# Performance work log

Measured on AMD Instinct MI355X. Metric: run time of the kernel, lower is better.

## Reference

```python
import jax, jax.numpy as jnp
import numpy as np

B, T, C, H = 8, 2048, 1024, 64  # batch, context_length, embedding_dim, head_size


def setup_inputs() -> dict:
    key = jax.random.key(0)
    kx, kq, kk, kv = jax.random.split(key, 4)
    s = C ** -0.5  # linear-init-like scale
    return {
        "x": jax.random.normal(kx, (B, T, C), dtype=jnp.float32),
        "Wq": jax.random.normal(kq, (C, H), dtype=jnp.float32) * s,
        "Wk": jax.random.normal(kk, (C, H), dtype=jnp.float32) * s,
        "Wv": jax.random.normal(kv, (C, H), dtype=jnp.float32) * s,
    }


def reference(x, Wq, Wk, Wv):
    Bx, Tx, _ = x.shape
    q = jnp.einsum('btc,ch->bth', x, Wq)
    k = jnp.einsum('btc,ch->bth', x, Wk)
    v = jnp.einsum('btc,ch->bth', x, Wv)
    scale = k.shape[-1] ** -0.5
    scores = jnp.einsum('bth,bsh->bts', q, k) * scale  # [B, T, T]
    causal = jnp.tril(jnp.ones((Tx, Tx), dtype=bool))
    scores = jnp.where(causal, scores, -jnp.inf)
    weights = jax.nn.softmax(scores, axis=-1)
    # dropout is identity in eval mode
    out = jnp.einsum('bts,bsh->bth', weights, v)  # [B, T, H]
    return out
```

## Files before the change

kernel.cpp:

```cpp
#include <hip/hip_runtime.h>
#include <hip/hip_bf16.h>

#define BB 8
#define TT 2048
#define CC 1024
#define HH 64

typedef float f32x4 __attribute__((ext_vector_type(4)));
typedef float f32x16 __attribute__((ext_vector_type(16)));
typedef short s16x8 __attribute__((ext_vector_type(8)));

static __device__ __forceinline__ unsigned short f2bf(float f) {
    unsigned int u = __float_as_uint(f);
    u = (u + 0x7FFFu + ((u >> 16) & 1u)) >> 16;
    return (unsigned short)u;
}

static __device__ __forceinline__ unsigned cvt_pk_bf16(float lo, float hi) {
    unsigned r;
    asm("v_cvt_pk_bf16_f32 %0, %1, %2" : "=v"(r) : "v"(lo), "v"(hi));
    return r;
}

__global__ __launch_bounds__(256) void wt_kernel(
    const float* __restrict__ Wq, const float* __restrict__ Wk,
    const float* __restrict__ Wv, unsigned short* __restrict__ wTf) {
    const int e8 = blockIdx.x * 256 + threadIdx.x;
    const int lane = e8 & 63;
    const int s = (e8 >> 6) & 31;
    const int n16 = e8 >> 11;
    const int sel = n16 >> 2;
    const float* W = (sel == 0) ? Wq : ((sel == 1) ? Wk : Wv);
    const int h = ((n16 & 3) << 4) + (lane & 15);
    const int cb = s * 32 + ((lane >> 4) << 3);
    s16x8 v;
#pragma unroll
    for (int j = 0; j < 8; ++j) v[j] = (short)f2bf(W[(size_t)(cb + j) * HH + h]);
    *reinterpret_cast<s16x8*>(&wTf[(size_t)e8 * 8]) = v;
}

__global__ __launch_bounds__(256, 2) void qkv_kernel(
    const float* __restrict__ x, const unsigned short* __restrict__ wTf,
    unsigned short* __restrict__ Qf, unsigned short* __restrict__ Kf,
    unsigned short* __restrict__ Vf) {
    __shared__ unsigned short xb[2][32 * 128];
    const int tid = threadIdx.x;
    const int wn = tid >> 6, lane = tid & 63;
    const int lo = lane & 15, hi = lane >> 4;
    const int rb = blockIdx.x * 32;

    const int r0 = tid >> 5;
    const int c4 = (tid & 31) * 4;
    const float* xsrc = &x[(size_t)(rb + r0) * CC + c4];

    const int ab0 = lo * 128, as0 = (lo & 7) << 3;
    const int ab1 = (16 + lo) * 128;

    f32x4 acc[2][3];
#pragma unroll
    for (int m = 0; m < 2; ++m)
#pragma unroll
        for (int n = 0; n < 3; ++n) acc[m][n] = (f32x4){0.f, 0.f, 0.f, 0.f};

    f32x4 pfA[4], pfB[4];
#pragma unroll
    for (int i = 0; i < 4; ++i)
        pfA[i] = *reinterpret_cast<const f32x4*>(xsrc + (size_t)(8 * i) * CC);
#pragma unroll
    for (int i = 0; i < 4; ++i)
        pfB[i] = *reinterpret_cast<const f32x4*>(xsrc + (size_t)(8 * i) * CC + 128);

    s16x8 bv[4][3];
#define BLOAD(SET, SLOT)                                                       \
    {                                                                          \
        _Pragma("unroll")                                                      \
        for (int n = 0; n < 3; ++n)                                            \
            bv[SET][n] = *reinterpret_cast<const s16x8*>(                      \
                &wTf[(((size_t)(wn * 3 + n) * 32 + (SLOT)) * 64 + lane) * 8]); \
    }
    BLOAD(0, 0)
    BLOAD(1, 1)
    BLOAD(2, 2)

#pragma unroll
    for (int c = 0; c < 8; ++c) {
        unsigned short* wb = xb[c & 1];
        {
            const f32x4* pf = (c & 1) ? pfB : pfA;
#pragma unroll
            for (int i = 0; i < 4; ++i) {
                const int rr = r0 + 8 * i;
                ushort4 g;
                g.x = f2bf(pf[i][0]); g.y = f2bf(pf[i][1]);
                g.z = f2bf(pf[i][2]); g.w = f2bf(pf[i][3]);
                *reinterpret_cast<ushort4*>(&wb[rr * 128 + (c4 ^ ((rr & 7) << 3))]) = g;
            }
        }
        __syncthreads();
        if (c < 6) {
            if (c & 1) {
#pragma unroll
                for (int i = 0; i < 4; ++i)
                    pfB[i] = *reinterpret_cast<const f32x4*>(
                        xsrc + (size_t)(8 * i) * CC + (c + 2) * 128);
            } else {
#pragma unroll
                for (int i = 0; i < 4; ++i)
                    pfA[i] = *reinterpret_cast<const f32x4*>(
                        xsrc + (size_t)(8 * i) * CC + (c + 2) * 128);
            }
        }
        const unsigned short* base = xb[c & 1];
#pragma unroll
        for (int kh = 0; kh < 4; ++kh) {
            const int slot = c * 4 + kh;
            if (slot + 3 < 32) BLOAD((slot + 3) & 3, slot + 3)
            const s16x8 a0 = *reinterpret_cast<const s16x8*>(
                &base[ab0 + ((kh * 32 + hi * 8) ^ as0)]);
            const s16x8 a1 = *reinterpret_cast<const s16x8*>(
                &base[ab1 + ((kh * 32 + hi * 8) ^ as0)]);
#pragma unroll
            for (int n = 0; n < 3; ++n) {
                acc[0][n] = __builtin_amdgcn_mfma_f32_16x16x32_bf16(a0, bv[slot & 3][n], acc[0][n], 0, 0, 0);
                acc[1][n] = __builtin_amdgcn_mfma_f32_16x16x32_bf16(a1, bv[slot & 3][n], acc[1][n], 0, 0, 0);
            }
        }
    }
#undef BLOAD

    __syncthreads();
    unsigned short* fr = reinterpret_cast<unsigned short*>(xb);
#pragma unroll
    for (int n = 0; n < 3; ++n) {
        const int n16 = wn * 3 + n;
        const int sel = n16 >> 2;
#pragma unroll
        for (int m = 0; m < 2; ++m) {
#pragma unroll
            for (int r = 0; r < 4; ++r) {
                const int tok31 = m * 16 + 4 * hi + r;
                const unsigned short bvv = f2bf(acc[m][n][r]);
                if (sel == 0) {
                    const int s = n16, half = (lo >> 3) & 1, j = lo & 7;
                    fr[(s * 64 + half * 32 + tok31) * 8 + j] = bvv;
                } else if (sel == 1) {
                    const int s = n16 - 4, half = (lo >> 3) & 1, j = lo & 7;
                    fr[2048 + (s * 64 + half * 32 + tok31) * 8 + j] = bvv;
                } else {
                    const int h = (n16 - 8) * 16 + lo;
                    const int mt = h >> 5;
                    const int s2 = tok31 >> 4, hf = (tok31 >> 3) & 1, jj = tok31 & 7;
                    fr[4096 + ((mt * 2 + s2) * 64 + hf * 32 + (h & 31)) * 8 + jj] = bvv;
                }
            }
        }
    }
    __syncthreads();
    const int b_ = rb >> 11;
    const int tile = (rb & (TT - 1)) >> 5;
    const size_t tb = ((size_t)b_ * 64 + tile) * 2048;
#pragma unroll
    for (int i = 0; i < 3; ++i) {
        const int g = tid + 256 * i;
        const int buf = g >> 8;
        const int off = g & 255;
        const s16x8 val = *reinterpret_cast<const s16x8*>(&fr[buf * 2048 + off * 8]);
        unsigned short* dst = (buf == 0) ? Qf : ((buf == 1) ? Kf : Vf);
        *reinterpret_cast<s16x8*>(&dst[tb + off * 8]) = val;
    }
}

__global__ __launch_bounds__(512, 4) void attn_kernel(
    const unsigned short* __restrict__ Qf, const unsigned short* __restrict__ Kf,
    const unsigned short* __restrict__ Vf, float* __restrict__ out) {
    __shared__ __align__(16) char smem[33792 + 2048];
    float (*OfL)[64][33] = reinterpret_cast<float(*)[64][33]>(smem);
    float (*Mm)[32] = reinterpret_cast<float(*)[32]>(smem + 33792);
    float (*Ml)[32] = reinterpret_cast<float(*)[32]>(smem + 33792 + 1024);

    const int tid = threadIdx.x;
    const int wv = tid >> 6, lane = tid & 63;
    const int q = lane & 31, half = lane >> 5;
    const int b = blockIdx.x & 7;
    const int qt = 63 - (blockIdx.x >> 3);
    const int qbase = qt * 32;
    const float CEXP = 0.125f * 1.44269504f;

    const unsigned short* qp = &Qf[(((size_t)b * 64 + qt) * 256 + lane) * 8];
    s16x8 qf[4];
#pragma unroll
    for (int s = 0; s < 4; ++s) qf[s] = *reinterpret_cast<const s16x8*>(qp + s * 512);

    f32x16 oA, oB;
#pragma unroll
    for (int r = 0; r < 16; ++r) { oA[r] = 0.f; oB[r] = 0.f; }
    float m = -1e30f, l = 0.f;

    for (int t = wv; t <= qt; t += 8) {
        const unsigned short* vp = &Vf[(((size_t)b * 64 + t) * 256 + lane) * 8];
        s16x8 vf[4];
#pragma unroll
        for (int i = 0; i < 4; ++i)
            vf[i] = *reinterpret_cast<const s16x8*>(vp + i * 512);
        const unsigned short* kp = &Kf[(((size_t)b * 64 + t) * 256 + lane) * 8];
        f32x16 sa;
#pragma unroll
        for (int r = 0; r < 16; ++r) sa[r] = 0.f;
#pragma unroll
        for (int s = 0; s < 4; ++s) {
            const s16x8 kf = *reinterpret_cast<const s16x8*>(kp + s * 512);
            sa = __builtin_amdgcn_mfma_f32_32x32x16_bf16(kf, qf[s], sa, 0, 0, 0);
        }
        if (t == qt) {
#pragma unroll
            for (int r = 0; r < 16; ++r) {
                const int key = 4 * half + (r & 3) + 8 * (r >> 2);
                if (key > q) sa[r] = -1e30f;
            }
        }
        float pmax = sa[0];
#pragma unroll
        for (int r = 1; r < 16; ++r) pmax = fmaxf(pmax, sa[r]);
        pmax = fmaxf(pmax, __shfl_xor(pmax, 32));
        if (!__all(pmax <= m + 64.f)) {
            const float mnew = fmaxf(m, pmax);
            const float alpha = exp2f((m - mnew) * CEXP);
            l *= alpha;
#pragma unroll
            for (int r = 0; r < 16; ++r) { oA[r] *= alpha; oB[r] *= alpha; }
            m = mnew;
        }
        float rs = 0.f;
#pragma unroll
        for (int r = 0; r < 16; ++r) {
            const float p = exp2f((sa[r] - m) * CEXP);
            sa[r] = p;
            rs += p;
        }
        l += rs + __shfl_xor(rs, 32);
        unsigned d[8];
#pragma unroll
        for (int i = 0; i < 8; ++i) d[i] = cvt_pk_bf16(sa[2 * i], sa[2 * i + 1]);
        const unsigned snd0 = half ? d[0] : d[2];
        const unsigned snd1 = half ? d[1] : d[3];
        const unsigned snd2 = half ? d[4] : d[6];
        const unsigned snd3 = half ? d[5] : d[7];
        const unsigned rcv0 = __shfl_xor(snd0, 32);
        const unsigned rcv1 = __shfl_xor(snd1, 32);
        const unsigned rcv2 = __shfl_xor(snd2, 32);
        const unsigned rcv3 = __shfl_xor(snd3, 32);
        union { unsigned u[4]; s16x8 v; } f0, f1;
        f0.u[0] = half ? rcv0 : d[0];
        f0.u[1] = half ? rcv1 : d[1];
        f0.u[2] = half ? d[2] : rcv0;
        f0.u[3] = half ? d[3] : rcv1;
        f1.u[0] = half ? rcv2 : d[4];
        f1.u[1] = half ? rcv3 : d[5];
        f1.u[2] = half ? d[6] : rcv2;
        f1.u[3] = half ? d[7] : rcv3;
        oA = __builtin_amdgcn_mfma_f32_32x32x16_bf16(vf[0], f0.v, oA, 0, 0, 0);
        oB = __builtin_amdgcn_mfma_f32_32x32x16_bf16(vf[2], f0.v, oB, 0, 0, 0);
        oA = __builtin_amdgcn_mfma_f32_32x32x16_bf16(vf[1], f1.v, oA, 0, 0, 0);
        oB = __builtin_amdgcn_mfma_f32_32x32x16_bf16(vf[3], f1.v, oB, 0, 0, 0);
    }

#define PUBLISH(slot)                                                      \
    {                                                                      \
        _Pragma("unroll")                                                  \
        for (int r = 0; r < 16; ++r) {                                     \
            const int h0 = (r & 3) + 8 * (r >> 2) + 4 * half;              \
            OfL[slot][h0][q] = oA[r];                                      \
            OfL[slot][h0 + 32][q] = oB[r];                                 \
        }                                                                  \
    }
#define MERGE(slot, srcw)                                                  \
    {                                                                      \
        const float mb = Mm[srcw][q], lb = Ml[srcw][q];                    \
        const float M = fmaxf(m, mb);                                      \
        const float wa = exp2f((m - M) * CEXP);                            \
        const float wb = exp2f((mb - M) * CEXP);                           \
        _Pragma("unroll")                                                  \
        for (int r = 0; r < 16; ++r) {                                     \
            const int h0 = (r & 3) + 8 * (r >> 2) + 4 * half;              \
            oA[r] = oA[r] * wa + OfL[slot][h0][q] * wb;                    \
            oB[r] = oB[r] * wa + OfL[slot][h0 + 32][q] * wb;               \
        }                                                                  \
        l = l * wa + lb * wb;                                              \
        m = M;                                                             \
    }

    if (lane < 32) { Mm[wv][q] = m; Ml[wv][q] = l; }
    if (wv >= 4) PUBLISH(wv - 4);
    __syncthreads();
    if (wv < 4) MERGE(wv, wv + 4);
    __syncthreads();
    if (wv == 2 || wv == 3) {
        PUBLISH(wv - 2);
        if (lane < 32) { Mm[wv][q] = m; Ml[wv][q] = l; }
    }
    __syncthreads();
    if (wv < 2) MERGE(wv, wv + 2);
    __syncthreads();
    if (wv == 1) {
        PUBLISH(1);
        if (lane < 32) { Mm[1][q] = m; Ml[1][q] = l; }
    }
    __syncthreads();
    if (wv == 0) {
        MERGE(1, 1);
        const float inv = 1.f / l;
#pragma unroll
        for (int r = 0; r < 16; ++r) {
            const int h0 = (r & 3) + 8 * (r >> 2) + 4 * half;
            OfL[0][h0][q] = oA[r] * inv;
            OfL[0][h0 + 32][q] = oB[r] * inv;
        }
    }
    __syncthreads();
#pragma unroll
    for (int i = 0; i < 4; ++i) {
        const int idx = tid + 512 * i;
        const int h = idx & 63, q2 = idx >> 6;
        out[((size_t)b * TT + qbase + q2) * HH + h] = OfL[0][h][q2];
    }
#undef PUBLISH
#undef MERGE
}

extern "C" void kernel_launch(void* const* d_in, const int* in_sizes, int n_in,
                              void* d_out, int out_size, void* d_ws, size_t ws_size,
                              hipStream_t stream) {
    (void)in_sizes; (void)n_in; (void)out_size; (void)ws_size;
    const float* x  = (const float*)d_in[0];
    const float* Wq = (const float*)d_in[1];
    const float* Wk = (const float*)d_in[2];
    const float* Wv = (const float*)d_in[3];
    float* out = (float*)d_out;

    char* ws = (char*)d_ws;
    unsigned short* wTf = (unsigned short*)ws;
    unsigned short* Qf  = (unsigned short*)(ws + 393216);
    unsigned short* Kf  = (unsigned short*)(ws + 393216 + 2097152);
    unsigned short* Vf  = (unsigned short*)(ws + 393216 + 4194304);

    wt_kernel<<<96, 256, 0, stream>>>(Wq, Wk, Wv, wTf);
    qkv_kernel<<<512, 256, 0, stream>>>(x, wTf, Qf, Kf, Vf);
    attn_kernel<<<512, 512, 0, stream>>>(Qf, Kf, Vf, out);
}
```

Before: 42.35 us.

## Load whole 32x1024 x tile into LDS upfront instead of double-buffered chunks

The QKV projection kernel now loads and converts the block's entire 32-row x slab (64 KB bf16 in LDS) in one pass with a single barrier, then runs all 32 MFMA k-slots without further barriers. This removes the per-chunk register prefetch, double-buffer switching and eight __syncthreads. In exchange, global-load latency is no longer overlapped with MFMA work, and the much larger LDS footprint may cut the number of resident blocks per CU below the launch-bounds target of 2.

```diff
diff --git a/kernel.cpp b/kernel.cpp
--- a/kernel.cpp
+++ b/kernel.cpp
@@ -43,32 +43,33 @@
     const float* __restrict__ x, const unsigned short* __restrict__ wTf,
     unsigned short* __restrict__ Qf, unsigned short* __restrict__ Kf,
     unsigned short* __restrict__ Vf) {
-    __shared__ unsigned short xb[2][32 * 128];
+    __shared__ unsigned short xt[32 * 1024];
     const int tid = threadIdx.x;
     const int wn = tid >> 6, lane = tid & 63;
     const int lo = lane & 15, hi = lane >> 4;
     const int rb = blockIdx.x * 32;
 
-    const int r0 = tid >> 5;
-    const int c4 = (tid & 31) * 4;
-    const float* xsrc = &x[(size_t)(rb + r0) * CC + c4];
-
-    const int ab0 = lo * 128, as0 = (lo & 7) << 3;
-    const int ab1 = (16 + lo) * 128;
+#pragma unroll
+    for (int i = 0; i < 16; ++i) {
+        const int gid = tid + 256 * i;
+        const int row = gid >> 7, g = gid & 127;
+        const float* src = &x[(size_t)(rb + row) * CC + g * 8];
+        const f32x4 f0 = *reinterpret_cast<const f32x4*>(src);
+        const f32x4 f1 = *reinterpret_cast<const f32x4*>(src + 4);
+        s16x8 w;
+        w[0] = (short)f2bf(f0[0]); w[1] = (short)f2bf(f0[1]);
+        w[2] = (short)f2bf(f0[2]); w[3] = (short)f2bf(f0[3]);
+        w[4] = (short)f2bf(f1[0]); w[5] = (short)f2bf(f1[1]);
+        w[6] = (short)f2bf(f1[2]); w[7] = (short)f2bf(f1[3]);
+        *reinterpret_cast<s16x8*>(&xt[row * 1024 + (g ^ (row & 7)) * 8]) = w;
+    }
+    __syncthreads();
 
     f32x4 acc[2][3];
 #pragma unroll
     for (int m = 0; m < 2; ++m)
 #pragma unroll
         for (int n = 0; n < 3; ++n) acc[m][n] = (f32x4){0.f, 0.f, 0.f, 0.f};
-
-    f32x4 pfA[4], pfB[4];
-#pragma unroll
-    for (int i = 0; i < 4; ++i)
-        pfA[i] = *reinterpret_cast<const f32x4*>(xsrc + (size_t)(8 * i) * CC);
-#pragma unroll
-    for (int i = 0; i < 4; ++i)
-        pfB[i] = *reinterpret_cast<const f32x4*>(xsrc + (size_t)(8 * i) * CC + 128);
 
     s16x8 bv[4][3];
 #define BLOAD(SET, SLOT)                                                       \
@@ -82,54 +83,25 @@
     BLOAD(1, 1)
     BLOAD(2, 2)
 
-#pragma unroll
-    for (int c = 0; c < 8; ++c) {
-        unsigned short* wb = xb[c & 1];
-        {
-            const f32x4* pf = (c & 1) ? pfB : pfA;
-#pragma unroll
-            for (int i = 0; i < 4; ++i) {
-                const int rr = r0 + 8 * i;
-                ushort4 g;
-                g.x = f2bf(pf[i][0]); g.y = f2bf(pf[i][1]);
-                g.z = f2bf(pf[i][2]); g.w = f2bf(pf[i][3]);
-                *reinterpret_cast<ushort4*>(&wb[rr * 128 + (c4 ^ ((rr & 7) << 3))]) = g;
-            }
-        }
-        __syncthreads();
-        if (c < 6) {
-            if (c & 1) {
-#pragma unroll
-                for (int i = 0; i < 4; ++i)
-                    pfB[i] = *reinterpret_cast<const f32x4*>(
-                        xsrc + (size_t)(8 * i) * CC + (c + 2) * 128);
-            } else {
-#pragma unroll
-                for (int i = 0; i < 4; ++i)
-                    pfA[i] = *reinterpret_cast<const f32x4*>(
-                        xsrc + (size_t)(8 * i) * CC + (c + 2) * 128);
-            }
-        }
-        const unsigned short* base = xb[c & 1];
-#pragma unroll
-        for (int kh = 0; kh < 4; ++kh) {
-            const int slot = c * 4 + kh;
-            if (slot + 3 < 32) BLOAD((slot + 3) & 3, slot + 3)
-            const s16x8 a0 = *reinterpret_cast<const s16x8*>(
-                &base[ab0 + ((kh * 32 + hi * 8) ^ as0)]);
-            const s16x8 a1 = *reinterpret_cast<const s16x8*>(
-                &base[ab1 + ((kh * 32 + hi * 8) ^ as0)]);
-#pragma unroll
-            for (int n = 0; n < 3; ++n) {
-                acc[0][n] = __builtin_amdgcn_mfma_f32_16x16x32_bf16(a0, bv[slot & 3][n], acc[0][n], 0, 0, 0);
-                acc[1][n] = __builtin_amdgcn_mfma_f32_16x16x32_bf16(a1, bv[slot & 3][n], acc[1][n], 0, 0, 0);
-            }
+    const int sw = lo & 7;
+#pragma unroll
+    for (int slot = 0; slot < 32; ++slot) {
+        if (slot + 3 < 32) BLOAD((slot + 3) & 3, slot + 3)
+        const int gr = slot * 4 + hi;
+        const s16x8 a0 = *reinterpret_cast<const s16x8*>(
+            &xt[lo * 1024 + (gr ^ sw) * 8]);
+        const s16x8 a1 = *reinterpret_cast<const s16x8*>(
+            &xt[(16 + lo) * 1024 + (gr ^ sw) * 8]);
+#pragma unroll
+        for (int n = 0; n < 3; ++n) {
+            acc[0][n] = __builtin_amdgcn_mfma_f32_16x16x32_bf16(a0, bv[slot & 3][n], acc[0][n], 0, 0, 0);
+            acc[1][n] = __builtin_amdgcn_mfma_f32_16x16x32_bf16(a1, bv[slot & 3][n], acc[1][n], 0, 0, 0);
         }
     }
 #undef BLOAD
 
     __syncthreads();
-    unsigned short* fr = reinterpret_cast<unsigned short*>(xb);
+    unsigned short* fr = xt;
 #pragma unroll
     for (int n = 0; n < 3; ++n) {
         const int n16 = wn * 3 + n;
```

Result: slower. 45.06 us (+6.4%).
